# Performance work log

Measured on AMD Instinct MI355X. Metric: run time of the kernel, lower is better.

The kernel has to match this reference:

```python
import jax, jax.numpy as jnp
import numpy as np

DIM = 768
N_HEADS = 12
HEAD_DIM = DIM // N_HEADS
HIDDEN = 4 * DIM
EPS = 1e-5


def _layernorm(x, gamma, beta):
    mu = jnp.mean(x, axis=-1, keepdims=True)
    var = jnp.mean(jnp.square(x - mu), axis=-1, keepdims=True)
    return (x - mu) * jax.lax.rsqrt(var + EPS) * gamma + beta


def setup_inputs() -> dict:
    key = jax.random.key(0)
    ks = jax.random.split(key, 8)
    B, N = 16, 1024
    s = 0.02
    return {
        "x": jax.random.normal(ks[0], (B, N, DIM), jnp.float32),
        "Wqkv": jax.random.normal(ks[1], (DIM, 3 * DIM), jnp.float32) * s,
        "bqkv": jnp.zeros((3 * DIM,), jnp.float32),
        "Wproj": jax.random.normal(ks[2], (DIM, DIM), jnp.float32) * s,
        "bproj": jnp.zeros((DIM,), jnp.float32),
        "g1": jnp.ones((DIM,), jnp.float32),
        "b1": jnp.zeros((DIM,), jnp.float32),
        "g2": jnp.ones((DIM,), jnp.float32),
        "b2": jnp.zeros((DIM,), jnp.float32),
        "W1": jax.random.normal(ks[3], (DIM, HIDDEN), jnp.float32) * s,
        "bf1": jnp.zeros((HIDDEN,), jnp.float32),
        "W2": jax.random.normal(ks[4], (HIDDEN, DIM), jnp.float32) * s,
        "bf2": jnp.zeros((DIM,), jnp.float32),
    }


def reference(x, Wqkv, bqkv, Wproj, bproj, g1, b1, g2, b2, W1, bf1, W2, bf2):
    B, N, _ = x.shape
    # --- attention branch (pre-LN) ---
    h = _layernorm(x, g1, b1)
    qkv = (h @ Wqkv + bqkv).reshape(B, N, 3, N_HEADS, HEAD_DIM)
    qkv = jnp.transpose(qkv, (2, 0, 3, 1, 4))  # [3, B, H, N, D]
    q, k, v = qkv[0], qkv[1], qkv[2]
    # NOTE: source scales by dim**-0.5, not head_dim**-0.5 (faithful)
    scores = jnp.einsum("bhnd,bhmd->bhnm", q, k) * (DIM ** -0.5)
    attn = jax.nn.softmax(scores, axis=-1)
    out = jnp.einsum("bhnm,bhmd->bhnd", attn, v)
    out = jnp.transpose(out, (0, 2, 1, 3)).reshape(B, N, DIM)
    x = x + (out @ Wproj + bproj)
    # --- MLP branch ---
    h2 = _layernorm(x, g2, b2)
    ff = jax.nn.relu(h2 @ W1 + bf1) @ W2 + bf2
    return x + ff
```

## Files before the change

### kernel.cpp

```cpp
#include <hip/hip_runtime.h>
#include <cstdint>
#include <cstddef>

typedef unsigned short u16;
typedef __bf16 bf16x8 __attribute__((ext_vector_type(8)));
typedef unsigned short u16x8 __attribute__((ext_vector_type(8)));
typedef float f32x4 __attribute__((ext_vector_type(4)));

#define DIMN 768
#define BNROWS 16384
#define NH 12
#define HD 64
#define HID 3072
#define QKVN 2304

__device__ __forceinline__ u16 f2bf(float f) {
  unsigned u = __builtin_bit_cast(unsigned, f);
  u += 0x7fffu + ((u >> 16) & 1u);
  return (u16)(u >> 16);
}

__device__ __forceinline__ bf16x8 ld8(const u16* p) {
  u16x8 v = *reinterpret_cast<const u16x8*>(p);
  return __builtin_bit_cast(bf16x8, v);
}

__device__ __forceinline__ void gload16(const void* g, void* l) {
  __builtin_amdgcn_global_load_lds(
      (const __attribute__((address_space(1))) unsigned int*)g,
      (__attribute__((address_space(3))) unsigned int*)l, 16, 0, 0);
}

#define MFMA(a, b, c) __builtin_amdgcn_mfma_f32_16x16x32_bf16(a, b, c, 0, 0, 0)

__global__ __launch_bounds__(256) void twb_k(const float* __restrict__ W,
                                             u16* __restrict__ Wt, int K, int N) {
  __shared__ float tile[32][33];
  const int n0 = blockIdx.x * 32, k0 = blockIdx.y * 32;
  const int tx = threadIdx.x & 31, ty = threadIdx.x >> 5;
#pragma unroll
  for (int i = 0; i < 4; i++)
    tile[ty + i * 8][tx] = W[(size_t)(k0 + ty + i * 8) * N + n0 + tx];
  __syncthreads();
#pragma unroll
  for (int i = 0; i < 4; i++)
    Wt[(size_t)(n0 + ty + i * 8) * K + k0 + tx] = f2bf(tile[tx][ty + i * 8]);
}

__global__ __launch_bounds__(256) void ln_k(const float* __restrict__ x,
                                            const float* __restrict__ g,
                                            const float* __restrict__ bta,
                                            u16* __restrict__ outp) {
  const int row = blockIdx.x * 4 + (threadIdx.x >> 6);
  const int lane = threadIdx.x & 63;
  const float4* xr = (const float4*)(x + (size_t)row * DIMN);
  float4 v[3];
  float s = 0.f, ss = 0.f;
#pragma unroll
  for (int c = 0; c < 3; c++) {
    v[c] = xr[c * 64 + lane];
    s += v[c].x + v[c].y + v[c].z + v[c].w;
    ss += v[c].x * v[c].x + v[c].y * v[c].y + v[c].z * v[c].z + v[c].w * v[c].w;
  }
#pragma unroll
  for (int off = 1; off < 64; off <<= 1) {
    s += __shfl_xor(s, off);
    ss += __shfl_xor(ss, off);
  }
  const float mu = s * (1.f / DIMN);
  const float var = ss * (1.f / DIMN) - mu * mu;
  const float rs = rsqrtf(var + 1e-5f);
  u16* orow = outp + (size_t)row * DIMN;
#pragma unroll
  for (int c = 0; c < 3; c++) {
    float4 gv = ((const float4*)g)[c * 64 + lane];
    float4 bv = ((const float4*)bta)[c * 64 + lane];
    ushort4 o;
    o.x = f2bf((v[c].x - mu) * rs * gv.x + bv.x);
    o.y = f2bf((v[c].y - mu) * rs * gv.y + bv.y);
    o.z = f2bf((v[c].z - mu) * rs * gv.z + bv.z);
    o.w = f2bf((v[c].w - mu) * rs * gv.w + bv.w);
    ((ushort4*)orow)[c * 64 + lane] = o;
  }
}

template <int OUT_BF16, int RELU, int RESID>
__global__ __launch_bounds__(512, 2) void gemm256_k(const u16* __restrict__ A,
                                                    const u16* __restrict__ Bt,
                                                    const float* __restrict__ bias,
                                                    const float* __restrict__ resid,
                                                    void* __restrict__ Cout, int N, int K) {
  __shared__ u16 lds[65536];
  const int tid = threadIdx.x;
  const int m0 = blockIdx.x * 256;
  const int n0 = blockIdx.y * 256;
  const int lane = tid & 63, w = tid >> 6;
  const int wr = w >> 2, wc = w & 3;
  const int lhi = lane >> 4, llo = lane & 15;
  const int NT = K >> 5;

  const int srow = tid >> 2, sc8 = (tid & 3) * 8;
  const u16* aS0 = A + (size_t)(m0 + srow) * K + sc8;
  const u16* aS1 = A + (size_t)(m0 + 128 + srow) * K + sc8;
  const u16* bS0 = Bt + (size_t)(n0 + srow) * K + sc8;
  const u16* bS1 = Bt + (size_t)(n0 + 128 + srow) * K + sc8;

  auto slotBase = [&](int t) -> char* { return (char*)lds + ((size_t)(t & 3) << 15); };
  auto stageA = [&](int t) {
    char* sb = slotBase(t);
    gload16(aS0 + t * 32, sb + tid * 16);
    gload16(aS1 + t * 32, sb + 8192 + tid * 16);
  };
  auto stageB = [&](int t) {
    char* sb = slotBase(t) + 16384;
    gload16(bS0 + t * 32, sb + tid * 16);
    gload16(bS1 + t * 32, sb + 8192 + tid * 16);
  };

  f32x4 acc[8][4] = {};

  stageA(0); stageB(0);
  stageA(1); stageB(1);
  stageA(2); stageB(2);
  asm volatile("s_waitcnt vmcnt(8)" ::: "memory");
  __builtin_amdgcn_s_barrier();

  for (int t = 0; t < NT; ++t) {
    const char* sb = slotBase(t);
    bf16x8 af[4], bfr[4];
#pragma unroll
    for (int ni = 0; ni < 4; ni++)
      bfr[ni] = ld8((const u16*)(sb + 16384 + (wc * 64 + ni * 16 + llo) * 64 + lhi * 16));
#pragma unroll
    for (int mi = 0; mi < 4; mi++)
      af[mi] = ld8((const u16*)(sb + (wr * 128 + mi * 16 + llo) * 64 + lhi * 16));
    if (t + 3 < NT) stageA(t + 3);
    __builtin_amdgcn_s_barrier();
    asm volatile("s_waitcnt lgkmcnt(0)" ::: "memory");
    __builtin_amdgcn_sched_barrier(0);
    __builtin_amdgcn_s_setprio(1);
#pragma unroll
    for (int mi = 0; mi < 4; mi++)
#pragma unroll
      for (int ni = 0; ni < 4; ni++) acc[mi][ni] = MFMA(af[mi], bfr[ni], acc[mi][ni]);
    __builtin_amdgcn_s_setprio(0);
    __builtin_amdgcn_sched_barrier(0);
    __builtin_amdgcn_s_barrier();
#pragma unroll
    for (int mi = 0; mi < 4; mi++)
      af[mi] = ld8((const u16*)(sb + (wr * 128 + 64 + mi * 16 + llo) * 64 + lhi * 16));
    if (t + 3 < NT) stageB(t + 3);
    __builtin_amdgcn_s_barrier();
    asm volatile("s_waitcnt lgkmcnt(0)" ::: "memory");
    __builtin_amdgcn_sched_barrier(0);
    __builtin_amdgcn_s_setprio(1);
#pragma unroll
    for (int mi = 0; mi < 4; mi++)
#pragma unroll
      for (int ni = 0; ni < 4; ni++) acc[4 + mi][ni] = MFMA(af[mi], bfr[ni], acc[4 + mi][ni]);
    __builtin_amdgcn_s_setprio(0);
    __builtin_amdgcn_sched_barrier(0);
    if (t + 3 < NT) {
      asm volatile("s_waitcnt vmcnt(8)" ::: "memory");
    } else if (t + 2 < NT) {
      asm volatile("s_waitcnt vmcnt(4)" ::: "memory");
    } else if (t + 1 < NT) {
      asm volatile("s_waitcnt vmcnt(0)" ::: "memory");
    }
    __builtin_amdgcn_s_barrier();
  }

#pragma unroll
  for (int mi = 0; mi < 8; mi++)
#pragma unroll
    for (int ni = 0; ni < 4; ni++) {
      const int row = m0 + wr * 128 + mi * 16 + lhi * 4;
      const int col = n0 + wc * 64 + ni * 16 + llo;
      const float bsv = bias[col];
#pragma unroll
      for (int rr = 0; rr < 4; rr++) {
        float v = acc[mi][ni][rr] + bsv;
        if (RELU) v = fmaxf(v, 0.0f);
        const size_t idx = (size_t)(row + rr) * N + col;
        if (RESID) v += resid[idx];
        if (OUT_BF16)
          ((u16*)Cout)[idx] = f2bf(v);
        else
          ((float*)Cout)[idx] = v;
      }
    }
}

__device__ __forceinline__ bf16x8 ldscale8(const u16* p, float c) {
  u16x8 v = *reinterpret_cast<const u16x8*>(p);
  bf16x8 r;
#pragma unroll
  for (int j = 0; j < 8; j++) {
    float f = __builtin_bit_cast(float, (unsigned)v[j] << 16) * c;
    r[j] = (__bf16)f;
  }
  return r;
}

__device__ __forceinline__ unsigned pack_bf2(float a, float b) {
  unsigned ua = (unsigned)__builtin_bit_cast(u16, (__bf16)a);
  unsigned ub = (unsigned)__builtin_bit_cast(u16, (__bf16)b);
  return ua | (ub << 16);
}

__global__ __launch_bounds__(256) void attn_k(const u16* __restrict__ qkv,
                                              u16* __restrict__ outp) {
  __shared__ u16 Ks[2][64 * 64];
  __shared__ u16 Vt[2][64 * 64];
  __shared__ u16 Ps[4][32 * 64];

  const int tid = threadIdx.x;
  const int f = blockIdx.x;
  const int bh = (f & 7) | ((f >> 6) << 3);
  const int qt = (f >> 3) & 7;
  const int b = bh / NH, h = bh - b * NH;
  const int lane = tid & 63, w = tid >> 6;
  const int lhi = lane >> 4, llo = lane & 15;
  const size_t rowb = (size_t)b * 1024;
  const int wq0 = qt * 128 + w * 32;
  const float SC = 0.052059750f;

  bf16x8 qb[2][2];
#pragma unroll
  for (int mi = 0; mi < 2; mi++) {
    const u16* qrow = qkv + (rowb + wq0 + mi * 16 + llo) * QKVN + h * HD;
    qb[mi][0] = ldscale8(qrow + lhi * 8, SC);
    qb[mi][1] = ldscale8(qrow + 32 + lhi * 8, SC);
  }

  const u16* kbase = qkv + rowb * QKVN + DIMN + h * HD;
  const u16* vbase = qkv + rowb * QKVN + 2 * DIMN + h * HD;
  const int vc8 = w * 8;
  const int sw = (llo & 7) * 8;
  const int rsw = llo & 7;

  const int srow = tid >> 3, su = tid & 7;
  const u16* ksrc = kbase + (size_t)srow * QKVN + (su ^ (srow & 7)) * 8;

  auto stageK = [&](int kt, int buf) {
    const u16* s0 = ksrc + (size_t)kt * 64 * QKVN;
    gload16(s0, (char*)&Ks[buf][0] + tid * 16);
    gload16(s0 + (size_t)32 * QKVN, (char*)&Ks[buf][0] + 4096 + tid * 16);
  };
  auto loadV = [&](int kt, u16x8& a, u16x8& c) {
    const u16* vr = vbase + (size_t)(kt * 64 + lane) * QKVN + vc8;
    a = *reinterpret_cast<const u16x8*>(vr);
    c = *reinterpret_cast<const u16x8*>(vr + 32);
  };
  auto writeV = [&](int buf, u16x8 a, u16x8 c) {
#pragma unroll
    for (int j = 0; j < 8; j++) {
      Vt[buf][(vc8 + j) * 64 + (lane ^ (j * 8))] = a[j];
      Vt[buf][(vc8 + 32 + j) * 64 + (lane ^ (j * 8))] = c[j];
    }
  };

  u16x8 v0, v1, nv0, nv1;

  stageK(0, 0);
  loadV(0, v0, v1);
  stageK(1, 1);
  asm volatile("s_waitcnt vmcnt(2)" ::: "memory");
  writeV(0, v0, v1);
  asm volatile("s_waitcnt lgkmcnt(0)" ::: "memory");
  __builtin_amdgcn_s_barrier();
  __builtin_amdgcn_sched_barrier(0);

  float psum[2] = {0.f, 0.f};
  f32x4 oacc[2][4] = {};

  for (int t = 0; t < 16; t++) {
    if (t < 15) loadV(t + 1, nv0, nv1);

    const u16* kB = &Ks[t & 1][0];
    f32x4 sacc[4][2] = {};
#pragma unroll
    for (int ks = 0; ks < 2; ks++)
#pragma unroll
      for (int ni = 0; ni < 4; ni++) {
        bf16x8 kf = ld8(&kB[(ni * 16 + llo) * 64 + (((ks * 4 + lhi) ^ rsw) * 8)]);
#pragma unroll
        for (int mi = 0; mi < 2; mi++) sacc[ni][mi] = MFMA(kf, qb[mi][ks], sacc[ni][mi]);
      }

    asm volatile("s_waitcnt lgkmcnt(0)" ::: "memory");
    __builtin_amdgcn_s_barrier();
    __builtin_amdgcn_sched_barrier(0);
    if (t + 2 < 16) stageK(t + 2, t & 1);

#pragma unroll
    for (int mi = 0; mi < 2; mi++)
#pragma unroll
      for (int ni = 0; ni < 4; ni++) {
        float p0 = __builtin_amdgcn_exp2f(sacc[ni][mi][0]);
        float p1 = __builtin_amdgcn_exp2f(sacc[ni][mi][1]);
        float p2 = __builtin_amdgcn_exp2f(sacc[ni][mi][2]);
        float p3 = __builtin_amdgcn_exp2f(sacc[ni][mi][3]);
        psum[mi] += (p0 + p1) + (p2 + p3);
        u16* pp = &Ps[w][(mi * 16 + llo) * 64 + ((ni * 16 + lhi * 4) ^ sw)];
        uint2 pw;
        pw.x = pack_bf2(p0, p1);
        pw.y = pack_bf2(p2, p3);
        *reinterpret_cast<uint2*>(pp) = pw;
      }

#pragma unroll
    for (int ks = 0; ks < 2; ks++) {
      const int koff = ks * 32 + lhi * 8;
      bf16x8 pa0 = ld8(&Ps[w][llo * 64 + (koff ^ sw)]);
      bf16x8 pa1 = ld8(&Ps[w][(16 + llo) * 64 + (koff ^ sw)]);
#pragma unroll
      for (int ni = 0; ni < 4; ni++) {
        bf16x8 vb = ld8(&Vt[t & 1][(ni * 16 + llo) * 64 + (koff ^ sw)]);
        oacc[0][ni] = MFMA(pa0, vb, oacc[0][ni]);
        oacc[1][ni] = MFMA(pa1, vb, oacc[1][ni]);
      }
    }

    if (t < 15) {
      if (t + 2 < 16) {
        asm volatile("s_waitcnt vmcnt(2)" ::: "memory");
      } else {
        asm volatile("s_waitcnt vmcnt(0)" ::: "memory");
      }
      writeV((t + 1) & 1, nv0, nv1);
      v0 = nv0; v1 = nv1;
      asm volatile("s_waitcnt lgkmcnt(0)" ::: "memory");
      __builtin_amdgcn_s_barrier();
      __builtin_amdgcn_sched_barrier(0);
    }
  }

  float rl[2][4];
#pragma unroll
  for (int mi = 0; mi < 2; mi++) {
    psum[mi] += __shfl_xor(psum[mi], 16);
    psum[mi] += __shfl_xor(psum[mi], 32);
#pragma unroll
    for (int r = 0; r < 4; r++) rl[mi][r] = 1.0f / __shfl(psum[mi], lhi * 4 + r);
  }

#pragma unroll
  for (int mi = 0; mi < 2; mi++)
#pragma unroll
    for (int ni = 0; ni < 4; ni++)
#pragma unroll
      for (int r = 0; r < 4; r++) {
        const size_t row = rowb + wq0 + mi * 16 + lhi * 4 + r;
        outp[row * DIMN + h * HD + ni * 16 + llo] = f2bf(oacc[mi][ni][r] * rl[mi][r]);
      }
}

extern "C" void kernel_launch(void* const* d_in, const int* in_sizes, int n_in,
                              void* d_out, int out_size, void* d_ws, size_t ws_size,
                              hipStream_t stream) {
  const float* x = (const float*)d_in[0];
  const float* Wqkv = (const float*)d_in[1];
  const float* bqkv = (const float*)d_in[2];
  const float* Wproj = (const float*)d_in[3];
  const float* bproj = (const float*)d_in[4];
  const float* g1 = (const float*)d_in[5];
  const float* b1 = (const float*)d_in[6];
  const float* g2 = (const float*)d_in[7];
  const float* b2 = (const float*)d_in[8];
  const float* W1 = (const float*)d_in[9];
  const float* bf1 = (const float*)d_in[10];
  const float* W2 = (const float*)d_in[11];
  const float* bf2 = (const float*)d_in[12];
  float* outp = (float*)d_out;

  char* p = (char*)d_ws;
  u16* WqkvT = (u16*)p; p += (size_t)QKVN * DIMN * 2;
  u16* WprojT = (u16*)p; p += (size_t)DIMN * DIMN * 2;
  u16* W1T = (u16*)p; p += (size_t)HID * DIMN * 2;
  u16* W2T = (u16*)p; p += (size_t)DIMN * HID * 2;
  u16* bufX = (u16*)p; p += (size_t)BNROWS * DIMN * 2;
  u16* big = (u16*)p; p += (size_t)BNROWS * HID * 2;

  twb_k<<<dim3(QKVN / 32, DIMN / 32), 256, 0, stream>>>(Wqkv, WqkvT, DIMN, QKVN);
  twb_k<<<dim3(DIMN / 32, DIMN / 32), 256, 0, stream>>>(Wproj, WprojT, DIMN, DIMN);
  twb_k<<<dim3(HID / 32, DIMN / 32), 256, 0, stream>>>(W1, W1T, DIMN, HID);
  twb_k<<<dim3(DIMN / 32, HID / 32), 256, 0, stream>>>(W2, W2T, HID, DIMN);

  ln_k<<<BNROWS / 4, 256, 0, stream>>>(x, g1, b1, bufX);
  gemm256_k<1, 0, 0><<<dim3(64, QKVN / 256), 512, 0, stream>>>(bufX, WqkvT, bqkv, nullptr,
                                                               big, QKVN, DIMN);
  attn_k<<<1536, 256, 0, stream>>>(big, bufX);
  gemm256_k<0, 0, 1><<<dim3(64, DIMN / 256), 512, 0, stream>>>(bufX, WprojT, bproj, x, outp,
                                                               DIMN, DIMN);
  ln_k<<<BNROWS / 4, 256, 0, stream>>>(outp, g2, b2, bufX);
  gemm256_k<1, 1, 0><<<dim3(64, HID / 256), 512, 0, stream>>>(bufX, W1T, bf1, nullptr, big,
                                                              HID, DIMN);
  gemm256_k<0, 0, 1><<<dim3(64, DIMN / 256), 512, 0, stream>>>(big, W2T, bf2, outp, outp,
                                                               DIMN, HID);
}
```

Before: 462.4 us.

## Add 256x128-tile GEMM for N=768 projections to raise block count

Adds a gemmP_k kernel with 256x128 output tiles, 256 threads (4 waves) and a 3-slot LDS ring that prefetches two tiles ahead in two half-stages. The output projection and second MLP GEMM (both N=768) switch to it, doubling the grid from 192 to 384 blocks to fill the device better. The trade-off is lower per-block reuse of A tiles, since each A row tile is now loaded by six blocks instead of three, which adds extra global traffic.

```diff
diff --git a/kernel.cpp b/kernel.cpp
--- a/kernel.cpp
+++ b/kernel.cpp
@@ -164,6 +164,111 @@
       asm volatile("s_waitcnt vmcnt(8)" ::: "memory");
     } else if (t + 2 < NT) {
       asm volatile("s_waitcnt vmcnt(4)" ::: "memory");
+    } else if (t + 1 < NT) {
+      asm volatile("s_waitcnt vmcnt(0)" ::: "memory");
+    }
+    __builtin_amdgcn_s_barrier();
+  }
+
+#pragma unroll
+  for (int mi = 0; mi < 8; mi++)
+#pragma unroll
+    for (int ni = 0; ni < 4; ni++) {
+      const int row = m0 + wr * 128 + mi * 16 + lhi * 4;
+      const int col = n0 + wc * 64 + ni * 16 + llo;
+      const float bsv = bias[col];
+#pragma unroll
+      for (int rr = 0; rr < 4; rr++) {
+        float v = acc[mi][ni][rr] + bsv;
+        if (RELU) v = fmaxf(v, 0.0f);
+        const size_t idx = (size_t)(row + rr) * N + col;
+        if (RESID) v += resid[idx];
+        if (OUT_BF16)
+          ((u16*)Cout)[idx] = f2bf(v);
+        else
+          ((float*)Cout)[idx] = v;
+      }
+    }
+}
+
+template <int OUT_BF16, int RELU, int RESID>
+__global__ __launch_bounds__(256, 2) void gemmP_k(const u16* __restrict__ A,
+                                                  const u16* __restrict__ Bt,
+                                                  const float* __restrict__ bias,
+                                                  const float* __restrict__ resid,
+                                                  void* __restrict__ Cout, int N, int K) {
+  __shared__ u16 lds[3 * 12288];
+  const int tid = threadIdx.x;
+  const int m0 = blockIdx.x * 256;
+  const int n0 = blockIdx.y * 128;
+  const int lane = tid & 63, w = tid >> 6;
+  const int wr = w >> 1, wc = w & 1;
+  const int lhi = lane >> 4, llo = lane & 15;
+  const int NT = K >> 5;
+
+  const int crow = tid >> 2, kc8 = (tid & 3) * 8;
+  const u16* aS = A + (size_t)(m0 + crow) * K + kc8;
+  const u16* bS = Bt + (size_t)(n0 + crow) * K + kc8;
+  const size_t a64 = (size_t)64 * K;
+
+  auto slotBase = [&](int t) -> char* { return (char*)lds + (t % 3) * 24576; };
+  auto stage1 = [&](int t) {
+    char* sb = slotBase(t);
+    gload16(aS + t * 32, sb + tid * 16);
+    gload16(aS + a64 + t * 32, sb + 4096 + tid * 16);
+    gload16(bS + t * 32, sb + 16384 + tid * 16);
+  };
+  auto stage2 = [&](int t) {
+    char* sb = slotBase(t);
+    gload16(aS + 2 * a64 + t * 32, sb + 8192 + tid * 16);
+    gload16(aS + 3 * a64 + t * 32, sb + 12288 + tid * 16);
+    gload16(bS + a64 + t * 32, sb + 16384 + 4096 + tid * 16);
+  };
+
+  f32x4 acc[8][4] = {};
+
+  stage1(0); stage2(0);
+  stage1(1); stage2(1);
+  asm volatile("s_waitcnt vmcnt(6)" ::: "memory");
+  __builtin_amdgcn_s_barrier();
+
+  for (int t = 0; t < NT; ++t) {
+    const char* sb = slotBase(t);
+    bf16x8 af[4], bfr[4];
+#pragma unroll
+    for (int ni = 0; ni < 4; ni++)
+      bfr[ni] = ld8((const u16*)(sb + 16384 + (wc * 64 + ni * 16 + llo) * 64 + lhi * 16));
+#pragma unroll
+    for (int mi = 0; mi < 4; mi++)
+      af[mi] = ld8((const u16*)(sb + (wr * 128 + mi * 16 + llo) * 64 + lhi * 16));
+    if (t + 2 < NT) stage1(t + 2);
+    __builtin_amdgcn_s_barrier();
+    asm volatile("s_waitcnt lgkmcnt(0)" ::: "memory");
+    __builtin_amdgcn_sched_barrier(0);
+    __builtin_amdgcn_s_setprio(1);
+#pragma unroll
+    for (int mi = 0; mi < 4; mi++)
+#pragma unroll
+      for (int ni = 0; ni < 4; ni++) acc[mi][ni] = MFMA(af[mi], bfr[ni], acc[mi][ni]);
+    __builtin_amdgcn_s_setprio(0);
+    __builtin_amdgcn_sched_barrier(0);
+    __builtin_amdgcn_s_barrier();
+#pragma unroll
+    for (int mi = 0; mi < 4; mi++)
+      af[mi] = ld8((const u16*)(sb + (wr * 128 + 64 + mi * 16 + llo) * 64 + lhi * 16));
+    if (t + 2 < NT) stage2(t + 2);
+    __builtin_amdgcn_s_barrier();
+    asm volatile("s_waitcnt lgkmcnt(0)" ::: "memory");
+    __builtin_amdgcn_sched_barrier(0);
+    __builtin_amdgcn_s_setprio(1);
+#pragma unroll
+    for (int mi = 0; mi < 4; mi++)
+#pragma unroll
+      for (int ni = 0; ni < 4; ni++) acc[4 + mi][ni] = MFMA(af[mi], bfr[ni], acc[4 + mi][ni]);
+    __builtin_amdgcn_s_setprio(0);
+    __builtin_amdgcn_sched_barrier(0);
+    if (t + 2 < NT) {
+      asm volatile("s_waitcnt vmcnt(6)" ::: "memory");
     } else if (t + 1 < NT) {
       asm volatile("s_waitcnt vmcnt(0)" ::: "memory");
     }
@@ -391,11 +496,11 @@
   gemm256_k<1, 0, 0><<<dim3(64, QKVN / 256), 512, 0, stream>>>(bufX, WqkvT, bqkv, nullptr,
                                                                big, QKVN, DIMN);
   attn_k<<<1536, 256, 0, stream>>>(big, bufX);
-  gemm256_k<0, 0, 1><<<dim3(64, DIMN / 256), 512, 0, stream>>>(bufX, WprojT, bproj, x, outp,
-                                                               DIMN, DIMN);
+  gemmP_k<0, 0, 1><<<dim3(64, DIMN / 128), 256, 0, stream>>>(bufX, WprojT, bproj, x, outp,
+                                                             DIMN, DIMN);
   ln_k<<<BNROWS / 4, 256, 0, stream>>>(outp, g2, b2, bufX);
   gemm256_k<1, 1, 0><<<dim3(64, HID / 256), 512, 0, stream>>>(bufX, W1T, bf1, nullptr, big,
                                                               HID, DIMN);
-  gemm256_k<0, 0, 1><<<dim3(64, DIMN / 256), 512, 0, stream>>>(big, W2T, bf2, outp, outp,
-                                                               DIMN, HID);
-}
+  gemmP_k<0, 0, 1><<<dim3(64, DIMN / 128), 256, 0, stream>>>(big, W2T, bf2, outp, outp,
+                                                             DIMN, HID);
+}
```

Result: no change. 455.8 us (-1.4%).
